# Kernel optimization log

Measured on AMD Instinct MI355X. Metric: run time of the kernel, lower is better.

The kernel has to match this reference:

```python
import jax, jax.numpy as jnp
import numpy as np

N_EMB = 64
N_HEAD = 8
HEAD = N_EMB // N_HEAD
BLOCK = 64
EPS = 1e-5


def setup_inputs() -> dict:
    key = jax.random.key(0)
    ks = jax.random.split(key, 12)
    B, T, C = 4096, 64, N_EMB
    s = 0.02
    return {
        "x": jax.random.normal(ks[0], (B, T, C), jnp.float32),
        "ln1_w": jnp.ones((C,), jnp.float32),
        "ln1_b": jnp.zeros((C,), jnp.float32),
        # stacked per-head projections, layout [H, C_in, head_size] (x @ W)
        "wq": jax.random.normal(ks[1], (N_HEAD, C, HEAD), jnp.float32) * s,
        "wk": jax.random.normal(ks[2], (N_HEAD, C, HEAD), jnp.float32) * s,
        "wv": jax.random.normal(ks[3], (N_HEAD, C, HEAD), jnp.float32) * s,
        "proj_w": jax.random.normal(ks[4], (C, C), jnp.float32) * s,
        "proj_b": jnp.zeros((C,), jnp.float32),
        "ln2_w": jnp.ones((C,), jnp.float32),
        "ln2_b": jnp.zeros((C,), jnp.float32),
        "fc1_w": jax.random.normal(ks[5], (C, 4 * C), jnp.float32) * s,
        "fc1_b": jnp.zeros((4 * C,), jnp.float32),
        "fc2_w": jax.random.normal(ks[6], (4 * C, C), jnp.float32) * s,
        "fc2_b": jnp.zeros((C,), jnp.float32),
    }


def _layernorm(x, w, b):
    mu = jnp.mean(x, axis=-1, keepdims=True)
    var = jnp.mean((x - mu) ** 2, axis=-1, keepdims=True)
    return (x - mu) * jax.lax.rsqrt(var + EPS) * w + b


def reference(x, ln1_w, ln1_b, wq, wk, wv, proj_w, proj_b,
              ln2_w, ln2_b, fc1_w, fc1_b, fc2_w, fc2_b):
    B, T, C = x.shape
    # --- self-attention branch (dropout in eval mode => identity) ---
    h = _layernorm(x, ln1_w, ln1_b)
    q = jnp.einsum("btc,hcd->bhtd", h, wq)
    k = jnp.einsum("btc,hcd->bhtd", h, wk)
    v = jnp.einsum("btc,hcd->bhtd", h, wv)
    # NOTE: original scales by C**-0.5 (full embed dim), not head_size**-0.5
    scores = jnp.einsum("bhtd,bhsd->bhts", q, k) * (C ** -0.5)
    causal = jnp.tril(jnp.ones((T, T), bool))
    scores = jnp.where(causal, scores, -jnp.inf)
    w = jax.nn.softmax(scores, axis=-1)
    attn = jnp.einsum("bhts,bhsd->bhtd", w, v)  # [B,H,T,hs]
    attn = attn.transpose(0, 2, 1, 3).reshape(B, T, C)  # concat heads
    x = x + attn @ proj_w + proj_b
    # --- feed-forward branch ---
    h2 = _layernorm(x, ln2_w, ln2_b)
    ff = jax.nn.relu(h2 @ fc1_w + fc1_b) @ fc2_w + fc2_b
    return x + ff
```

## Files before the change

kernel.cpp:

```cpp
#include <hip/hip_runtime.h>

typedef __attribute__((ext_vector_type(8))) short bf16x8;
typedef __attribute__((ext_vector_type(4))) float f32x4;
typedef __attribute__((ext_vector_type(2))) unsigned int u32x2;
typedef __attribute__((ext_vector_type(4))) unsigned int u32x4;

__device__ __forceinline__ unsigned short f2bf(float f) {
  return __builtin_bit_cast(unsigned short, (__bf16)f);
}
__device__ __forceinline__ unsigned pk2(float a, float b) {
  return (unsigned)f2bf(a) | ((unsigned)f2bf(b) << 16);
}
__device__ __forceinline__ float bf2f(unsigned short h) {
  unsigned u = ((unsigned)h) << 16;
  return __builtin_bit_cast(float, u);
}
__device__ __forceinline__ bf16x8 frag(u32x4 v) { return __builtin_bit_cast(bf16x8, v); }

#if __has_builtin(__builtin_amdgcn_exp2f)
#define EXP2(x) __builtin_amdgcn_exp2f(x)
#else
#define EXP2(x) exp2f(x)
#endif

__device__ __forceinline__ void wfence() {
  asm volatile("" ::: "memory");
  __builtin_amdgcn_wave_barrier();
}
__device__ __forceinline__ void sfence() { __builtin_amdgcn_sched_barrier(0); }

#define MFMA16(a, b, c) __builtin_amdgcn_mfma_f32_16x16x32_bf16(a, b, c, 0, 0, 0)

#define LR 72
#define OFF_VT 4608
#define OFF_Q  9216
#define ZROW   13824
#define OFF_WST 13904
#define LDS_TOT (13904 + 12288)

#define WS_X2 65536

__global__ void prep_weights(const float* __restrict__ wq, const float* __restrict__ wk,
                             const float* __restrict__ wv, const float* __restrict__ projw,
                             const float* __restrict__ fc1w, const float* __restrict__ fc2w,
                             unsigned short* __restrict__ ws) {
  int c = blockIdx.x * 4 + (threadIdx.x >> 6), l = threadIdx.x & 63;
  int g = l >> 4, jl = l & 15;
  int kind, T, ks;
  if (c < 8)       { kind = 0; T = c >> 1;        ks = c & 1; }
  else if (c < 16) { kind = 1; T = (c - 8) >> 1;  ks = (c - 8) & 1; }
  else if (c < 24) { kind = 2; T = (c - 16) >> 1; ks = (c - 16) & 1; }
  else if (c < 32) { kind = 3; T = (c - 24) >> 1; ks = (c - 24) & 1; }
  else if (c < 64) { kind = 4; T = (c - 32) >> 1; ks = (c - 32) & 1; }
  else             { kind = 5; T = (c - 64) >> 3; ks = (c - 64) & 7; }
  int n = 16 * T + jl;
  unsigned short* dst = ws + c * 512 + l * 8;
  #pragma unroll
  for (int jj = 0; jj < 8; ++jj) {
    int kp = 16 * (2 * (ks & 1) + (jj >> 2)) + 4 * g + (jj & 3);
    int kn = 32 * ks + 8 * g + jj;
    float v;
    if (kind == 0)      v = wq[(n >> 3) * 512 + kp * 8 + (n & 7)] * 0.18033688011f;
    else if (kind == 1) v = wk[(n >> 3) * 512 + kp * 8 + (n & 7)];
    else if (kind == 2) v = wv[(n >> 3) * 512 + kp * 8 + (n & 7)];
    else if (kind == 3) v = projw[kn * 64 + n];
    else if (kind == 4) v = fc1w[kp * 256 + n];
    else                v = fc2w[(64 * (ks >> 1) + kp) * 64 + n];
    dst[jj] = f2bf(v);
  }
}

__global__ __launch_bounds__(256, 3) void block_attn(
    const float* __restrict__ x,
    const float* __restrict__ ln1w, const float* __restrict__ ln1b,
    const float* __restrict__ projb,
    unsigned short* __restrict__ wsm) {
  __shared__ __attribute__((aligned(16))) unsigned short lds[LDS_TOT];

  const int tid  = threadIdx.x;
  const int w    = tid >> 6;
  const int lane = tid & 63;
  const int g    = lane >> 4;
  const int jl   = lane & 15;
  const size_t b = blockIdx.x;
  const float* xb = x + b * 4096;
  const f32x4 zf = {0.f, 0.f, 0.f, 0.f};

  const int myrow = 16 * w + jl;
  const int krow  = myrow * LR;
  const int qrow  = OFF_Q + myrow * LR;
  const int sigb  = 32 * (w >> 1) + 8 * g + 4 * (w & 1);

  const u32x4* wsrc = (const u32x4*)wsm;
  u32x4 stg0 = wsrc[0 * 256 + tid], stg1 = wsrc[1 * 256 + tid];
  u32x4 stg2 = wsrc[2 * 256 + tid], stg3 = wsrc[3 * 256 + tid];
  u32x4 stg4 = wsrc[4 * 256 + tid], stg5 = wsrc[5 * 256 + tid];

  f32x4 xw[4];
  float mean, rstd;
  unsigned hr[8];
  {
    float s = 0.f, ss = 0.f;
    #pragma unroll
    for (int mi = 0; mi < 4; ++mi) {
      xw[mi] = *(const f32x4*)(xb + myrow * 64 + 16 * mi + 4 * g);
      #pragma unroll
      for (int r = 0; r < 4; ++r) { s += xw[mi][r]; ss += xw[mi][r] * xw[mi][r]; }
    }
    s  += __shfl_xor(s, 16, 64);  s  += __shfl_xor(s, 32, 64);
    ss += __shfl_xor(ss, 16, 64); ss += __shfl_xor(ss, 32, 64);
    mean = s * 0.015625f;
    rstd = rsqrtf(ss * 0.015625f - mean * mean + 1e-5f);
    #pragma unroll
    for (int mi = 0; mi < 4; ++mi) {
      f32x4 lw = *(const f32x4*)(ln1w + 16 * mi + 4 * g);
      f32x4 lb = *(const f32x4*)(ln1b + 16 * mi + 4 * g);
      float o0 = (xw[mi][0] - mean) * rstd * lw[0] + lb[0];
      float o1 = (xw[mi][1] - mean) * rstd * lw[1] + lb[1];
      float o2 = (xw[mi][2] - mean) * rstd * lw[2] + lb[2];
      float o3 = (xw[mi][3] - mean) * rstd * lw[3] + lb[3];
      hr[2 * mi] = pk2(o0, o1); hr[2 * mi + 1] = pk2(o2, o3);
    }
  }
  bf16x8 hb0 = frag((u32x4){hr[0], hr[1], hr[2], hr[3]});
  bf16x8 hb1 = frag((u32x4){hr[4], hr[5], hr[6], hr[7]});

  {
    u32x4* wdst = (u32x4*)(lds + OFF_WST);
    wdst[0 * 256 + tid] = stg0; wdst[1 * 256 + tid] = stg1;
    wdst[2 * 256 + tid] = stg2; wdst[3 * 256 + tid] = stg3;
    wdst[4 * 256 + tid] = stg4; wdst[5 * 256 + tid] = stg5;
  }
  if (tid < 40) ((unsigned*)(lds + ZROW))[tid] = 0u;
  __syncthreads();

  #pragma clang loop unroll(disable)
  for (int mt = 0; mt < 4; ++mt) {
    const unsigned short* wq8 = lds + OFF_WST + (2 * mt) * 512 + lane * 8;
    bf16x8 aq0 = *(const bf16x8*)(wq8);
    bf16x8 aq1 = *(const bf16x8*)(wq8 + 512);
    bf16x8 ak0 = *(const bf16x8*)(wq8 + 8 * 512);
    bf16x8 ak1 = *(const bf16x8*)(wq8 + 9 * 512);
    bf16x8 bv0 = *(const bf16x8*)(wq8 + 16 * 512);
    bf16x8 bv1 = *(const bf16x8*)(wq8 + 17 * 512);
    f32x4 q = MFMA16(aq0, hb0, zf); q = MFMA16(aq1, hb1, q);
    *(u32x2*)(lds + qrow + 16 * mt + 4 * g) = (u32x2){pk2(q[0], q[1]), pk2(q[2], q[3])};
    f32x4 kk = MFMA16(ak0, hb0, zf); kk = MFMA16(ak1, hb1, kk);
    *(u32x2*)(lds + krow + 16 * mt + 4 * g) = (u32x2){pk2(kk[0], kk[1]), pk2(kk[2], kk[3])};
    f32x4 vv = MFMA16(hb0, bv0, zf); vv = MFMA16(hb1, bv1, vv);
    *(u32x2*)(lds + OFF_VT + (16 * mt + jl) * LR + sigb) =
        (u32x2){pk2(vv[0], vv[1]), pk2(vv[2], vv[3])};
  }
  __syncthreads();

  {
    const bool g0 = (g == 0), j8 = (jl < 8);
    const int ka0 = g0 ? ((0  + jl) * LR) : ZROW;
    const int ka1 = g0 ? ((16 + jl) * LR) : ZROW;
    const int ka2 = g0 ? ((32 + jl) * LR) : ZROW;
    const int ka3 = g0 ? ((48 + jl) * LR) : ZROW;
    const int qb0 = g0 ? (OFF_Q + (0  + jl) * LR) : ZROW;
    const int qb1 = g0 ? (OFF_Q + (16 + jl) * LR) : ZROW;
    const int qb2 = g0 ? (OFF_Q + (32 + jl) * LR) : ZROW;
    const int qb3 = g0 ? (OFF_Q + (48 + jl) * LR) : ZROW;
    const bool m0 = (4 * g + 0 <= jl), m1 = (4 * g + 1 <= jl);
    const bool m2 = (4 * g + 2 <= jl), m3 = (4 * g + 3 <= jl);
    #pragma clang loop unroll(disable)
    for (int hh = 0; hh < 2; ++hh) {
      const int ho = 16 * w + 8 * hh;
      const int vbase = j8 ? (OFF_VT + (ho + jl) * LR) : ZROW;
      bf16x8 bq0 = *(const bf16x8*)(lds + qb0 + ho);
      bf16x8 bq1 = *(const bf16x8*)(lds + qb1 + ho);
      bf16x8 bq2 = *(const bf16x8*)(lds + qb2 + ho);
      bf16x8 bq3 = *(const bf16x8*)(lds + qb3 + ho);
      bf16x8 k0  = *(const bf16x8*)(lds + ka0 + ho);
      bf16x8 k1  = *(const bf16x8*)(lds + ka1 + ho);
      bf16x8 k2  = *(const bf16x8*)(lds + ka2 + ho);
      bf16x8 k3  = *(const bf16x8*)(lds + ka3 + ho);
      bf16x8 aw0 = *(const bf16x8*)(lds + vbase + 8 * g);
      bf16x8 aw1 = *(const bf16x8*)(lds + vbase + 32 + 8 * g);
      wfence();
      f32x4 s00 = MFMA16(k0, bq0, zf);
      f32x4 s10 = MFMA16(k0, bq1, zf);
      f32x4 s11 = MFMA16(k1, bq1, zf);
      {
        float e0 = m0 ? EXP2(s00[0]) : 0.f, e1 = m1 ? EXP2(s00[1]) : 0.f;
        float e2 = m2 ? EXP2(s00[2]) : 0.f, e3 = m3 ? EXP2(s00[3]) : 0.f;
        float sum = (e0 + e1) + (e2 + e3);
        sum += __shfl_xor(sum, 16, 64); sum += __shfl_xor(sum, 32, 64);
        float inv = __builtin_amdgcn_rcpf(sum);
        bf16x8 bp0 = frag((u32x4){pk2(e0, e1), pk2(e2, e3), 0u, 0u});
        f32x4 pv = MFMA16(aw0, bp0, zf);
        if (g < 2)
          *(u32x2*)(lds + OFF_Q + jl * LR + ho + 4 * g) =
              (u32x2){pk2(pv[0] * inv, pv[1] * inv), pk2(pv[2] * inv, pv[3] * inv)};
      }
      {
        float a0 = EXP2(s10[0]), a1 = EXP2(s10[1]);
        float a2 = EXP2(s10[2]), a3 = EXP2(s10[3]);
        float e0 = m0 ? EXP2(s11[0]) : 0.f, e1 = m1 ? EXP2(s11[1]) : 0.f;
        float e2 = m2 ? EXP2(s11[2]) : 0.f, e3 = m3 ? EXP2(s11[3]) : 0.f;
        float sum = ((a0 + a1) + (a2 + a3)) + ((e0 + e1) + (e2 + e3));
        sum += __shfl_xor(sum, 16, 64); sum += __shfl_xor(sum, 32, 64);
        float inv = __builtin_amdgcn_rcpf(sum);
        bf16x8 bp0 = frag((u32x4){pk2(a0, a1), pk2(a2, a3), pk2(e0, e1), pk2(e2, e3)});
        f32x4 pv = MFMA16(aw0, bp0, zf);
        if (g < 2)
          *(u32x2*)(lds + OFF_Q + (16 + jl) * LR + ho + 4 * g) =
              (u32x2){pk2(pv[0] * inv, pv[1] * inv), pk2(pv[2] * inv, pv[3] * inv)};
      }
      f32x4 s20 = MFMA16(k0, bq2, zf);
      f32x4 s21 = MFMA16(k1, bq2, zf);
      f32x4 s22 = MFMA16(k2, bq2, zf);
      f32x4 s30 = MFMA16(k0, bq3, zf);
      f32x4 s31 = MFMA16(k1, bq3, zf);
      f32x4 s32 = MFMA16(k2, bq3, zf);
      f32x4 s33 = MFMA16(k3, bq3, zf);
      {
        float a0 = EXP2(s20[0]), a1 = EXP2(s20[1]);
        float a2 = EXP2(s20[2]), a3 = EXP2(s20[3]);
        float c0 = EXP2(s21[0]), c1 = EXP2(s21[1]);
        float c2 = EXP2(s21[2]), c3 = EXP2(s21[3]);
        float e0 = m0 ? EXP2(s22[0]) : 0.f, e1 = m1 ? EXP2(s22[1]) : 0.f;
        float e2 = m2 ? EXP2(s22[2]) : 0.f, e3 = m3 ? EXP2(s22[3]) : 0.f;
        float sum = ((a0 + a1) + (a2 + a3)) + ((c0 + c1) + (c2 + c3))
                  + ((e0 + e1) + (e2 + e3));
        sum += __shfl_xor(sum, 16, 64); sum += __shfl_xor(sum, 32, 64);
        float inv = __builtin_amdgcn_rcpf(sum);
        bf16x8 bp0 = frag((u32x4){pk2(a0, a1), pk2(a2, a3), pk2(c0, c1), pk2(c2, c3)});
        bf16x8 bp1 = frag((u32x4){pk2(e0, e1), pk2(e2, e3), 0u, 0u});
        f32x4 pv = MFMA16(aw0, bp0, zf); pv = MFMA16(aw1, bp1, pv);
        if (g < 2)
          *(u32x2*)(lds + OFF_Q + (32 + jl) * LR + ho + 4 * g) =
              (u32x2){pk2(pv[0] * inv, pv[1] * inv), pk2(pv[2] * inv, pv[3] * inv)};
      }
      {
        float a0 = EXP2(s30[0]), a1 = EXP2(s30[1]);
        float a2 = EXP2(s30[2]), a3 = EXP2(s30[3]);
        float c0 = EXP2(s31[0]), c1 = EXP2(s31[1]);
        float c2 = EXP2(s31[2]), c3 = EXP2(s31[3]);
        float d0 = EXP2(s32[0]), d1 = EXP2(s32[1]);
        float d2 = EXP2(s32[2]), d3 = EXP2(s32[3]);
        float e0 = m0 ? EXP2(s33[0]) : 0.f, e1 = m1 ? EXP2(s33[1]) : 0.f;
        float e2 = m2 ? EXP2(s33[2]) : 0.f, e3 = m3 ? EXP2(s33[3]) : 0.f;
        float sum = ((a0 + a1) + (a2 + a3)) + ((c0 + c1) + (c2 + c3))
                  + ((d0 + d1) + (d2 + d3)) + ((e0 + e1) + (e2 + e3));
        sum += __shfl_xor(sum, 16, 64); sum += __shfl_xor(sum, 32, 64);
        float inv = __builtin_amdgcn_rcpf(sum);
        bf16x8 bp0 = frag((u32x4){pk2(a0, a1), pk2(a2, a3), pk2(c0, c1), pk2(c2, c3)});
        bf16x8 bp1 = frag((u32x4){pk2(d0, d1), pk2(d2, d3), pk2(e0, e1), pk2(e2, e3)});
        f32x4 pv = MFMA16(aw0, bp0, zf); pv = MFMA16(aw1, bp1, pv);
        if (g < 2)
          *(u32x2*)(lds + OFF_Q + (48 + jl) * LR + ho + 4 * g) =
              (u32x2){pk2(pv[0] * inv, pv[1] * inv), pk2(pv[2] * inv, pv[3] * inv)};
      }
    }
  }
  __syncthreads();
  bf16x8 bat0 = *(const bf16x8*)(lds + qrow + 8 * g);
  bf16x8 bat1 = *(const bf16x8*)(lds + qrow + 32 + 8 * g);

  {
    unsigned short* xrow = wsm + WS_X2 + (b * 64 + (size_t)myrow) * 64;
    f32x4 x20, x21, x22, x23;
    {
      bf16x8 a0 = *(const bf16x8*)(wsm + 24 * 512 + lane * 8);
      bf16x8 a1 = *(const bf16x8*)(wsm + 25 * 512 + lane * 8);
      f32x4 acc = MFMA16(a0, bat0, zf); acc = MFMA16(a1, bat1, acc);
      x20 = xw[0] + acc + *(const f32x4*)(projb + 4 * g);
    }
    {
      bf16x8 a0 = *(const bf16x8*)(wsm + 26 * 512 + lane * 8);
      bf16x8 a1 = *(const bf16x8*)(wsm + 27 * 512 + lane * 8);
      f32x4 acc = MFMA16(a0, bat0, zf); acc = MFMA16(a1, bat1, acc);
      x21 = xw[1] + acc + *(const f32x4*)(projb + 16 + 4 * g);
    }
    *(u32x4*)(xrow + 8 * g) = (u32x4){pk2(x20[0], x20[1]), pk2(x20[2], x20[3]),
                                      pk2(x21[0], x21[1]), pk2(x21[2], x21[3])};
    {
      bf16x8 a0 = *(const bf16x8*)(wsm + 28 * 512 + lane * 8);
      bf16x8 a1 = *(const bf16x8*)(wsm + 29 * 512 + lane * 8);
      f32x4 acc = MFMA16(a0, bat0, zf); acc = MFMA16(a1, bat1, acc);
      x22 = xw[2] + acc + *(const f32x4*)(projb + 32 + 4 * g);
    }
    {
      bf16x8 a0 = *(const bf16x8*)(wsm + 30 * 512 + lane * 8);
      bf16x8 a1 = *(const bf16x8*)(wsm + 31 * 512 + lane * 8);
      f32x4 acc = MFMA16(a0, bat0, zf); acc = MFMA16(a1, bat1, acc);
      x23 = xw[3] + acc + *(const f32x4*)(projb + 48 + 4 * g);
    }
    *(u32x4*)(xrow + 32 + 8 * g) = (u32x4){pk2(x22[0], x22[1]), pk2(x22[2], x22[3]),
                                           pk2(x23[0], x23[1]), pk2(x23[2], x23[3])};
  }
}

__global__ __launch_bounds__(256, 2) void ff_stream(
    const unsigned short* __restrict__ wsm,
    const float* __restrict__ ln2w, const float* __restrict__ ln2b,
    const float* __restrict__ fc1b, const float* __restrict__ fc2b,
    float* __restrict__ out) {
  __shared__ __attribute__((aligned(16))) unsigned short ldsw[32768];

  const int tid  = threadIdx.x;
  const int w    = tid >> 6;
  const int lane = tid & 63;
  const int g    = lane >> 4;
  const int jl   = lane & 15;
  const int myrow = 16 * w + jl;
  const f32x4 zf = {0.f, 0.f, 0.f, 0.f};

  {
    const u32x4* src = (const u32x4*)(wsm + 16384);
    u32x4* dst = (u32x4*)ldsw;
    #pragma unroll
    for (int k = 0; k < 16; ++k) dst[k * 256 + tid] = src[k * 256 + tid];
  }
  __syncthreads();

  f32x4 lw2[4], lb2[4], fb2[4];
  #pragma unroll
  for (int mi = 0; mi < 4; ++mi) {
    lw2[mi] = *(const f32x4*)(ln2w + 16 * mi + 4 * g);
    lb2[mi] = *(const f32x4*)(ln2b + 16 * mi + 4 * g);
    fb2[mi] = *(const f32x4*)(fc2b + 16 * mi + 4 * g);
  }

  const unsigned short* x2g = wsm + WS_X2;
  const size_t tbase = (size_t)blockIdx.x * 512 + myrow;

  u32x4 v0 = *(const u32x4*)(x2g + tbase * 64 + 8 * g);
  u32x4 v1 = *(const u32x4*)(x2g + tbase * 64 + 32 + 8 * g);

  #pragma clang loop unroll(disable)
  for (int p = 0; p < 8; ++p) {
    const size_t t = tbase + p * 64;
    f32x4 x2[4];
    #pragma unroll
    for (int q = 0; q < 2; ++q) {
      u32x4 vv = q ? v1 : v0;
      x2[2 * q + 0][0] = bf2f((unsigned short)(vv[0] & 0xFFFF));
      x2[2 * q + 0][1] = bf2f((unsigned short)(vv[0] >> 16));
      x2[2 * q + 0][2] = bf2f((unsigned short)(vv[1] & 0xFFFF));
      x2[2 * q + 0][3] = bf2f((unsigned short)(vv[1] >> 16));
      x2[2 * q + 1][0] = bf2f((unsigned short)(vv[2] & 0xFFFF));
      x2[2 * q + 1][1] = bf2f((unsigned short)(vv[2] >> 16));
      x2[2 * q + 1][2] = bf2f((unsigned short)(vv[3] & 0xFFFF));
      x2[2 * q + 1][3] = bf2f((unsigned short)(vv[3] >> 16));
    }
    if (p < 7) {
      v0 = *(const u32x4*)(x2g + (t + 64) * 64 + 8 * g);
      v1 = *(const u32x4*)(x2g + (t + 64) * 64 + 32 + 8 * g);
    }
    sfence();

    float s = 0.f, ss = 0.f;
    #pragma unroll
    for (int mi = 0; mi < 4; ++mi)
      #pragma unroll
      for (int r = 0; r < 4; ++r) { s += x2[mi][r]; ss += x2[mi][r] * x2[mi][r]; }
    s  += __shfl_xor(s, 16, 64);  s  += __shfl_xor(s, 32, 64);
    ss += __shfl_xor(ss, 16, 64); ss += __shfl_xor(ss, 32, 64);
    float mean2 = s * 0.015625f;
    float rstd2 = rsqrtf(ss * 0.015625f - mean2 * mean2 + 1e-5f);
    unsigned h2[8];
    #pragma unroll
    for (int mi = 0; mi < 4; ++mi) {
      float o0 = (x2[mi][0] - mean2) * rstd2 * lw2[mi][0] + lb2[mi][0];
      float o1 = (x2[mi][1] - mean2) * rstd2 * lw2[mi][1] + lb2[mi][1];
      float o2 = (x2[mi][2] - mean2) * rstd2 * lw2[mi][2] + lb2[mi][2];
      float o3 = (x2[mi][3] - mean2) * rstd2 * lw2[mi][3] + lb2[mi][3];
      h2[2 * mi] = pk2(o0, o1); h2[2 * mi + 1] = pk2(o2, o3);
    }
    bf16x8 hc0 = frag((u32x4){h2[0], h2[1], h2[2], h2[3]});
    bf16x8 hc1 = frag((u32x4){h2[4], h2[5], h2[6], h2[7]});

    f32x4 acc2[4];
    #pragma unroll
    for (int mi = 0; mi < 4; ++mi) acc2[mi] = zf;
    #pragma clang loop unroll(disable)
    for (int c = 0; c < 4; ++c) {
      const unsigned short* w1c = ldsw + (8 * c) * 512 + lane * 8;
      const unsigned short* w2c = ldsw + (32 + 2 * c) * 512 + lane * 8;
      const float* b1c = fc1b + 64 * c + 4 * g;
      unsigned fr0, fr1, fr2, fr3, fr4, fr5, fr6, fr7;
      {
        bf16x8 a0 = *(const bf16x8*)(w1c);
        bf16x8 a1 = *(const bf16x8*)(w1c + 512);
        f32x4 acc = MFMA16(a0, hc0, zf); acc = MFMA16(a1, hc1, acc);
        f32x4 bb = *(const f32x4*)(b1c);
        fr0 = pk2(fmaxf(acc[0] + bb[0], 0.f), fmaxf(acc[1] + bb[1], 0.f));
        fr1 = pk2(fmaxf(acc[2] + bb[2], 0.f), fmaxf(acc[3] + bb[3], 0.f));
      }
      {
        bf16x8 a0 = *(const bf16x8*)(w1c + 2 * 512);
        bf16x8 a1 = *(const bf16x8*)(w1c + 3 * 512);
        f32x4 acc = MFMA16(a0, hc0, zf); acc = MFMA16(a1, hc1, acc);
        f32x4 bb = *(const f32x4*)(b1c + 16);
        fr2 = pk2(fmaxf(acc[0] + bb[0], 0.f), fmaxf(acc[1] + bb[1], 0.f));
        fr3 = pk2(fmaxf(acc[2] + bb[2], 0.f), fmaxf(acc[3] + bb[3], 0.f));
      }
      {
        bf16x8 a0 = *(const bf16x8*)(w1c + 4 * 512);
        bf16x8 a1 = *(const bf16x8*)(w1c + 5 * 512);
        f32x4 acc = MFMA16(a0, hc0, zf); acc = MFMA16(a1, hc1, acc);
        f32x4 bb = *(const f32x4*)(b1c + 32);
        fr4 = pk2(fmaxf(acc[0] + bb[0], 0.f), fmaxf(acc[1] + bb[1], 0.f));
        fr5 = pk2(fmaxf(acc[2] + bb[2], 0.f), fmaxf(acc[3] + bb[3], 0.f));
      }
      {
        bf16x8 a0 = *(const bf16x8*)(w1c + 6 * 512);
        bf16x8 a1 = *(const bf16x8*)(w1c + 7 * 512);
        f32x4 acc = MFMA16(a0, hc0, zf); acc = MFMA16(a1, hc1, acc);
        f32x4 bb = *(const f32x4*)(b1c + 48);
        fr6 = pk2(fmaxf(acc[0] + bb[0], 0.f), fmaxf(acc[1] + bb[1], 0.f));
        fr7 = pk2(fmaxf(acc[2] + bb[2], 0.f), fmaxf(acc[3] + bb[3], 0.f));
      }
      bf16x8 bf0 = frag((u32x4){fr0, fr1, fr2, fr3});
      bf16x8 bf1 = frag((u32x4){fr4, fr5, fr6, fr7});
      #pragma unroll
      for (int mi = 0; mi < 4; ++mi) {
        bf16x8 w20 = *(const bf16x8*)(w2c + (8 * mi) * 512);
        bf16x8 w21 = *(const bf16x8*)(w2c + (8 * mi + 1) * 512);
        acc2[mi] = MFMA16(w20, bf0, acc2[mi]);
        acc2[mi] = MFMA16(w21, bf1, acc2[mi]);
      }
    }
    float* ob = out + t * 64;
    #pragma unroll
    for (int mi = 0; mi < 4; ++mi) {
      f32x4 o = x2[mi] + acc2[mi] + fb2[mi];
      *(f32x4*)(ob + 16 * mi + 4 * g) = o;
    }
  }
}

extern "C" void kernel_launch(void* const* d_in, const int* in_sizes, int n_in,
                              void* d_out, int out_size, void* d_ws, size_t ws_size,
                              hipStream_t stream) {
  const float* x     = (const float*)d_in[0];
  const float* ln1w  = (const float*)d_in[1];
  const float* ln1b  = (const float*)d_in[2];
  const float* wq    = (const float*)d_in[3];
  const float* wk    = (const float*)d_in[4];
  const float* wvp   = (const float*)d_in[5];
  const float* projw = (const float*)d_in[6];
  const float* projb = (const float*)d_in[7];
  const float* ln2w  = (const float*)d_in[8];
  const float* ln2b  = (const float*)d_in[9];
  const float* fc1w  = (const float*)d_in[10];
  const float* fc1b  = (const float*)d_in[11];
  const float* fc2w  = (const float*)d_in[12];
  const float* fc2b  = (const float*)d_in[13];
  unsigned short* ws = (unsigned short*)d_ws;
  float* out = (float*)d_out;

  prep_weights<<<dim3(24), dim3(256), 0, stream>>>(wq, wk, wvp, projw, fc1w, fc2w, ws);

  int nblk = in_sizes[0] / 4096;
  block_attn<<<dim3(nblk), dim3(256), 0, stream>>>(
      x, ln1w, ln1b, projb, ws);

  int nblk2 = (nblk * 64) / 512;
  ff_stream<<<dim3(nblk2), dim3(256), 0, stream>>>(ws, ln2w, ln2b, fc1b, fc2b, out);
}
```

Before: 82.09 us.

## Process four token groups per FFN iteration to reuse LDS weight fragments

The FFN loop now handles four 16-token groups per iteration (two iterations instead of eight). Each fc1/fc2 weight fragment read from LDS is reused across four MFMA groups, and prefetching grows to four groups at a time. This cuts LDS weight reads per token and gives more independent MFMAs to interleave. In exchange it needs many more VGPRs for accumulators and x2 values, which can lower occupancy or cause spills.

```diff
diff --git a/kernel.cpp b/kernel.cpp
--- a/kernel.cpp
+++ b/kernel.cpp
@@ -328,108 +328,114 @@
   const unsigned short* x2g = wsm + WS_X2;
   const size_t tbase = (size_t)blockIdx.x * 512 + myrow;
 
-  u32x4 v0 = *(const u32x4*)(x2g + tbase * 64 + 8 * g);
-  u32x4 v1 = *(const u32x4*)(x2g + tbase * 64 + 32 + 8 * g);
+  u32x4 v0[4], v1[4];
+  #pragma unroll
+  for (int gi = 0; gi < 4; ++gi) {
+    v0[gi] = *(const u32x4*)(x2g + (tbase + 64 * gi) * 64 + 8 * g);
+    v1[gi] = *(const u32x4*)(x2g + (tbase + 64 * gi) * 64 + 32 + 8 * g);
+  }
 
   #pragma clang loop unroll(disable)
-  for (int p = 0; p < 8; ++p) {
-    const size_t t = tbase + p * 64;
-    f32x4 x2[4];
-    #pragma unroll
-    for (int q = 0; q < 2; ++q) {
-      u32x4 vv = q ? v1 : v0;
-      x2[2 * q + 0][0] = bf2f((unsigned short)(vv[0] & 0xFFFF));
-      x2[2 * q + 0][1] = bf2f((unsigned short)(vv[0] >> 16));
-      x2[2 * q + 0][2] = bf2f((unsigned short)(vv[1] & 0xFFFF));
-      x2[2 * q + 0][3] = bf2f((unsigned short)(vv[1] >> 16));
-      x2[2 * q + 1][0] = bf2f((unsigned short)(vv[2] & 0xFFFF));
-      x2[2 * q + 1][1] = bf2f((unsigned short)(vv[2] >> 16));
-      x2[2 * q + 1][2] = bf2f((unsigned short)(vv[3] & 0xFFFF));
-      x2[2 * q + 1][3] = bf2f((unsigned short)(vv[3] >> 16));
-    }
-    if (p < 7) {
-      v0 = *(const u32x4*)(x2g + (t + 64) * 64 + 8 * g);
-      v1 = *(const u32x4*)(x2g + (t + 64) * 64 + 32 + 8 * g);
+  for (int p = 0; p < 2; ++p) {
+    const size_t tp = tbase + p * 256;
+    f32x4 x2[4][4];
+    #pragma unroll
+    for (int gi = 0; gi < 4; ++gi)
+      #pragma unroll
+      for (int q = 0; q < 2; ++q) {
+        u32x4 vv = q ? v1[gi] : v0[gi];
+        #pragma unroll
+        for (int h = 0; h < 2; ++h) {
+          x2[gi][2 * q + h][0] = bf2f((unsigned short)(vv[2 * h] & 0xFFFF));
+          x2[gi][2 * q + h][1] = bf2f((unsigned short)(vv[2 * h] >> 16));
+          x2[gi][2 * q + h][2] = bf2f((unsigned short)(vv[2 * h + 1] & 0xFFFF));
+          x2[gi][2 * q + h][3] = bf2f((unsigned short)(vv[2 * h + 1] >> 16));
+        }
+      }
+    if (p < 1) {
+      #pragma unroll
+      for (int gi = 0; gi < 4; ++gi) {
+        v0[gi] = *(const u32x4*)(x2g + (tp + 256 + 64 * gi) * 64 + 8 * g);
+        v1[gi] = *(const u32x4*)(x2g + (tp + 256 + 64 * gi) * 64 + 32 + 8 * g);
+      }
     }
     sfence();
 
-    float s = 0.f, ss = 0.f;
-    #pragma unroll
-    for (int mi = 0; mi < 4; ++mi)
-      #pragma unroll
-      for (int r = 0; r < 4; ++r) { s += x2[mi][r]; ss += x2[mi][r] * x2[mi][r]; }
-    s  += __shfl_xor(s, 16, 64);  s  += __shfl_xor(s, 32, 64);
-    ss += __shfl_xor(ss, 16, 64); ss += __shfl_xor(ss, 32, 64);
-    float mean2 = s * 0.015625f;
-    float rstd2 = rsqrtf(ss * 0.015625f - mean2 * mean2 + 1e-5f);
-    unsigned h2[8];
-    #pragma unroll
-    for (int mi = 0; mi < 4; ++mi) {
-      float o0 = (x2[mi][0] - mean2) * rstd2 * lw2[mi][0] + lb2[mi][0];
-      float o1 = (x2[mi][1] - mean2) * rstd2 * lw2[mi][1] + lb2[mi][1];
-      float o2 = (x2[mi][2] - mean2) * rstd2 * lw2[mi][2] + lb2[mi][2];
-      float o3 = (x2[mi][3] - mean2) * rstd2 * lw2[mi][3] + lb2[mi][3];
-      h2[2 * mi] = pk2(o0, o1); h2[2 * mi + 1] = pk2(o2, o3);
-    }
-    bf16x8 hc0 = frag((u32x4){h2[0], h2[1], h2[2], h2[3]});
-    bf16x8 hc1 = frag((u32x4){h2[4], h2[5], h2[6], h2[7]});
-
-    f32x4 acc2[4];
-    #pragma unroll
-    for (int mi = 0; mi < 4; ++mi) acc2[mi] = zf;
+    bf16x8 hc0[4], hc1[4];
+    #pragma unroll
+    for (int gi = 0; gi < 4; ++gi) {
+      float s = 0.f, ss = 0.f;
+      #pragma unroll
+      for (int mi = 0; mi < 4; ++mi)
+        #pragma unroll
+        for (int r = 0; r < 4; ++r) { s += x2[gi][mi][r]; ss += x2[gi][mi][r] * x2[gi][mi][r]; }
+      s  += __shfl_xor(s, 16, 64);  s  += __shfl_xor(s, 32, 64);
+      ss += __shfl_xor(ss, 16, 64); ss += __shfl_xor(ss, 32, 64);
+      float m = s * 0.015625f;
+      float r = rsqrtf(ss * 0.015625f - m * m + 1e-5f);
+      unsigned h2[8];
+      #pragma unroll
+      for (int mi = 0; mi < 4; ++mi) {
+        float o0 = (x2[gi][mi][0] - m) * r * lw2[mi][0] + lb2[mi][0];
+        float o1 = (x2[gi][mi][1] - m) * r * lw2[mi][1] + lb2[mi][1];
+        float o2 = (x2[gi][mi][2] - m) * r * lw2[mi][2] + lb2[mi][2];
+        float o3 = (x2[gi][mi][3] - m) * r * lw2[mi][3] + lb2[mi][3];
+        h2[2 * mi] = pk2(o0, o1); h2[2 * mi + 1] = pk2(o2, o3);
+      }
+      hc0[gi] = frag((u32x4){h2[0], h2[1], h2[2], h2[3]});
+      hc1[gi] = frag((u32x4){h2[4], h2[5], h2[6], h2[7]});
+    }
+
+    f32x4 acc[4][4];
+    #pragma unroll
+    for (int gi = 0; gi < 4; ++gi)
+      #pragma unroll
+      for (int mi = 0; mi < 4; ++mi) acc[gi][mi] = zf;
     #pragma clang loop unroll(disable)
     for (int c = 0; c < 4; ++c) {
       const unsigned short* w1c = ldsw + (8 * c) * 512 + lane * 8;
       const unsigned short* w2c = ldsw + (32 + 2 * c) * 512 + lane * 8;
       const float* b1c = fc1b + 64 * c + 4 * g;
-      unsigned fr0, fr1, fr2, fr3, fr4, fr5, fr6, fr7;
+      bf16x8 bf0[4], bf1[4];
       {
-        bf16x8 a0 = *(const bf16x8*)(w1c);
-        bf16x8 a1 = *(const bf16x8*)(w1c + 512);
-        f32x4 acc = MFMA16(a0, hc0, zf); acc = MFMA16(a1, hc1, acc);
-        f32x4 bb = *(const f32x4*)(b1c);
-        fr0 = pk2(fmaxf(acc[0] + bb[0], 0.f), fmaxf(acc[1] + bb[1], 0.f));
-        fr1 = pk2(fmaxf(acc[2] + bb[2], 0.f), fmaxf(acc[3] + bb[3], 0.f));
-      }
-      {
-        bf16x8 a0 = *(const bf16x8*)(w1c + 2 * 512);
-        bf16x8 a1 = *(const bf16x8*)(w1c + 3 * 512);
-        f32x4 acc = MFMA16(a0, hc0, zf); acc = MFMA16(a1, hc1, acc);
-        f32x4 bb = *(const f32x4*)(b1c + 16);
-        fr2 = pk2(fmaxf(acc[0] + bb[0], 0.f), fmaxf(acc[1] + bb[1], 0.f));
-        fr3 = pk2(fmaxf(acc[2] + bb[2], 0.f), fmaxf(acc[3] + bb[3], 0.f));
-      }
-      {
-        bf16x8 a0 = *(const bf16x8*)(w1c + 4 * 512);
-        bf16x8 a1 = *(const bf16x8*)(w1c + 5 * 512);
-        f32x4 acc = MFMA16(a0, hc0, zf); acc = MFMA16(a1, hc1, acc);
-        f32x4 bb = *(const f32x4*)(b1c + 32);
-        fr4 = pk2(fmaxf(acc[0] + bb[0], 0.f), fmaxf(acc[1] + bb[1], 0.f));
-        fr5 = pk2(fmaxf(acc[2] + bb[2], 0.f), fmaxf(acc[3] + bb[3], 0.f));
-      }
-      {
-        bf16x8 a0 = *(const bf16x8*)(w1c + 6 * 512);
-        bf16x8 a1 = *(const bf16x8*)(w1c + 7 * 512);
-        f32x4 acc = MFMA16(a0, hc0, zf); acc = MFMA16(a1, hc1, acc);
-        f32x4 bb = *(const f32x4*)(b1c + 48);
-        fr6 = pk2(fmaxf(acc[0] + bb[0], 0.f), fmaxf(acc[1] + bb[1], 0.f));
-        fr7 = pk2(fmaxf(acc[2] + bb[2], 0.f), fmaxf(acc[3] + bb[3], 0.f));
-      }
-      bf16x8 bf0 = frag((u32x4){fr0, fr1, fr2, fr3});
-      bf16x8 bf1 = frag((u32x4){fr4, fr5, fr6, fr7});
+        unsigned fr[4][8];
+        #pragma unroll
+        for (int ml = 0; ml < 4; ++ml) {
+          bf16x8 a0 = *(const bf16x8*)(w1c + (2 * ml) * 512);
+          bf16x8 a1 = *(const bf16x8*)(w1c + (2 * ml + 1) * 512);
+          f32x4 bb = *(const f32x4*)(b1c + 16 * ml);
+          #pragma unroll
+          for (int gi = 0; gi < 4; ++gi) {
+            f32x4 t = MFMA16(a0, hc0[gi], zf); t = MFMA16(a1, hc1[gi], t);
+            fr[gi][2 * ml]     = pk2(fmaxf(t[0] + bb[0], 0.f), fmaxf(t[1] + bb[1], 0.f));
+            fr[gi][2 * ml + 1] = pk2(fmaxf(t[2] + bb[2], 0.f), fmaxf(t[3] + bb[3], 0.f));
+          }
+        }
+        #pragma unroll
+        for (int gi = 0; gi < 4; ++gi) {
+          bf0[gi] = frag((u32x4){fr[gi][0], fr[gi][1], fr[gi][2], fr[gi][3]});
+          bf1[gi] = frag((u32x4){fr[gi][4], fr[gi][5], fr[gi][6], fr[gi][7]});
+        }
+      }
       #pragma unroll
       for (int mi = 0; mi < 4; ++mi) {
         bf16x8 w20 = *(const bf16x8*)(w2c + (8 * mi) * 512);
         bf16x8 w21 = *(const bf16x8*)(w2c + (8 * mi + 1) * 512);
-        acc2[mi] = MFMA16(w20, bf0, acc2[mi]);
-        acc2[mi] = MFMA16(w21, bf1, acc2[mi]);
-      }
-    }
-    float* ob = out + t * 64;
-    #pragma unroll
-    for (int mi = 0; mi < 4; ++mi) {
-      f32x4 o = x2[mi] + acc2[mi] + fb2[mi];
-      *(f32x4*)(ob + 16 * mi + 4 * g) = o;
+        #pragma unroll
+        for (int gi = 0; gi < 4; ++gi) {
+          acc[gi][mi] = MFMA16(w20, bf0[gi], acc[gi][mi]);
+          acc[gi][mi] = MFMA16(w21, bf1[gi], acc[gi][mi]);
+        }
+      }
+    }
+    #pragma unroll
+    for (int gi = 0; gi < 4; ++gi) {
+      float* ob = out + (tp + 64 * gi) * 64;
+      #pragma unroll
+      for (int mi = 0; mi < 4; ++mi) {
+        f32x4 o = x2[gi][mi] + acc[gi][mi] + fb2[mi];
+        *(f32x4*)(ob + 16 * mi + 4 * g) = o;
+      }
     }
   }
 }
```

After: 96.86 us. +18.0%, slower.
